# Kernel optimization log

Hardware: AMD Instinct MI355X
Metric: run time of the kernel (lower is better)

Reference implementation:

```python
import jax, jax.numpy as jnp
import numpy as np

SCALE = 1.0 / 8.0  # source divides sim_M by literal 8 (== sqrt(d_k=64))


def setup_inputs() -> dict:
    key = jax.random.key(0)
    ks = jax.random.split(key, 7)
    B, S, D = 16, 2048, 512  # D = n_head * d_k = 8 * 64
    s = 1.0 / np.sqrt(D)
    return {
        "x": jax.random.normal(ks[0], (B, S, D), dtype=jnp.float32),
        "Wq": jax.random.normal(ks[1], (D, D), dtype=jnp.float32) * s,
        "bq": jax.random.normal(ks[2], (D,), dtype=jnp.float32) * 0.01,
        "Wk": jax.random.normal(ks[3], (D, D), dtype=jnp.float32) * s,
        "bk": jax.random.normal(ks[4], (D,), dtype=jnp.float32) * 0.01,
        "Wv": jax.random.normal(ks[5], (D, D), dtype=jnp.float32) * s,
        "bv": jax.random.normal(ks[6], (D,), dtype=jnp.float32) * 0.01,
    }


def reference(x, Wq, bq, Wk, bk, Wv, bv):
    # Manual QKV projections (no head split, matching the source code)
    q = jnp.einsum("bsd,de->bse", x, Wq) + bq  # [B,S,D]
    k = jnp.einsum("bsd,de->bse", x, Wk) + bk  # [B,S,D]
    v = jnp.einsum("bsd,de->bse", x, Wv) + bv  # [B,S,D]
    # bmm -> softmax -> bmm attention
    sim = jnp.einsum("bqe,bke->bqk", q, k) * SCALE  # [B,S,S]
    attn = jax.nn.softmax(sim, axis=-1)
    out = jnp.einsum("bqk,bkd->bqd", attn, v)  # [B,S,D]
    return out
```

## Files before the change

kernel.cpp:

```cpp
#include <hip/hip_runtime.h>
#include <math.h>

typedef _Float16 f16;
typedef _Float16 f16x2 __attribute__((ext_vector_type(2)));
typedef _Float16 f16x8 __attribute__((ext_vector_type(8)));
typedef float f32x4 __attribute__((ext_vector_type(4)));

#define NB 16
#define SS 2048
#define DD 512

__device__ __forceinline__ void gl_lds16(const void* g, void* l) {
  __builtin_amdgcn_global_load_lds(
      (const __attribute__((address_space(1))) unsigned int*)g,
      (__attribute__((address_space(3))) unsigned int*)l, 16, 0, 0);
}

__device__ __forceinline__ int pk2(float a, float b) {
  f16x2 t = {(f16)a, (f16)b};
  return __builtin_bit_cast(int, t);
}

__global__ __launch_bounds__(256) void cast_kernel(const float* __restrict__ x,
                                                   f16* __restrict__ o) {
  size_t i = (size_t)blockIdx.x * 256 + threadIdx.x;
  const float4* p = (const float4*)x + i * 2;
  float4 a = p[0], b = p[1];
  f16x8 v = {(f16)a.x, (f16)a.y, (f16)a.z, (f16)a.w,
             (f16)b.x, (f16)b.y, (f16)b.z, (f16)b.w};
  *((f16x8*)o + i) = v;
}

__global__ __launch_bounds__(256) void transpose_kernel(
    const float* __restrict__ W0, const float* __restrict__ W1,
    const float* __restrict__ W2, f16* __restrict__ T0, f16* __restrict__ T1,
    f16* __restrict__ T2) {
  const float* W = (blockIdx.z == 0) ? W0 : (blockIdx.z == 1) ? W1 : W2;
  f16* Wt = (blockIdx.z == 0) ? T0 : (blockIdx.z == 1) ? T1 : T2;
  __shared__ float t[32][33];
  int bx = blockIdx.x * 32, by = blockIdx.y * 32;
  int c = threadIdx.x & 31, r0 = threadIdx.x >> 5;
  for (int r = r0; r < 32; r += 8) t[r][c] = W[(size_t)(by + r) * DD + bx + c];
  __syncthreads();
  for (int r = r0; r < 32; r += 8) Wt[(size_t)(bx + r) * DD + by + c] = (f16)t[c][r];
}

__global__ __launch_bounds__(256) void gemm3_kernel(
    const f16* __restrict__ xh, const f16* __restrict__ WqT,
    const f16* __restrict__ WkT, const f16* __restrict__ WvT,
    f16* __restrict__ Qh, f16* __restrict__ Kh, f16* __restrict__ Vth,
    const float* __restrict__ bq, const float* __restrict__ bk,
    const float* __restrict__ bv) {
  const int wid = (blockIdx.x & 7) * 384 + (blockIdx.x >> 3);
  const f16* A;
  const f16* Bt;
  f16* C;
  const float* bias;
  int m0, n0, ldc, bias_row;
  float scale;
  if (wid < 2048) {
    const bool isK = wid >= 1024;
    const int r = wid & 1023;
    A = xh;
    Bt = isK ? WkT : WqT;
    C = isK ? Kh : Qh;
    bias = isK ? bk : bq;
    m0 = (r >> 2) * 128;
    n0 = (r & 3) * 128;
    ldc = DD;
    bias_row = 0;
    scale = isK ? 1.0f : 0.125f;
  } else {
    const int v = wid - 2048;
    const int bz = v >> 6, xy = v & 63;
    A = WvT;
    Bt = xh + (size_t)bz * SS * DD;
    C = Vth + (size_t)bz * (size_t)DD * SS;
    bias = bv;
    m0 = ((xy >> 4) & 3) * 128;
    n0 = (xy & 15) * 128;
    ldc = SS;
    bias_row = 1;
    scale = 1.0f;
  }
  __shared__ f16 Ash[2][128 * 32];
  __shared__ f16 Bsh[2][128 * 32];
  const int tid = threadIdx.x, lane = tid & 63, wave = tid >> 6;
  const int wm = wave & 1, wn = wave >> 1;
  const int l15 = lane & 15, lq = lane >> 4;
  f32x4 acc[4][4] = {};
  const int srow = tid >> 2, part = tid & 3;
  const f16* gA = A + (size_t)(m0 + srow) * DD + part * 8;
  const f16* gB = Bt + (size_t)(n0 + srow) * DD + part * 8;
  auto stage = [&](int sb, int kt) {
    f16* lA = &Ash[sb][tid * 8];
    f16* lB = &Bsh[sb][tid * 8];
    gl_lds16(gA + kt * 32, lA);
    gl_lds16(gA + 64 * DD + kt * 32, lA + 2048);
    gl_lds16(gB + kt * 32, lB);
    gl_lds16(gB + 64 * DD + kt * 32, lB + 2048);
  };
  stage(0, 0);
  __syncthreads();
  for (int kt = 0; kt < 16; ++kt) {
    const int buf = kt & 1;
    if (kt < 15) stage(buf ^ 1, kt + 1);
    f16x8 af[4], bf[4];
#pragma unroll
    for (int i = 0; i < 4; ++i)
      af[i] = *(const f16x8*)&Ash[buf][(64 * wm + 16 * i + l15) * 32 + lq * 8];
#pragma unroll
    for (int j = 0; j < 4; ++j)
      bf[j] = *(const f16x8*)&Bsh[buf][(64 * wn + 16 * j + l15) * 32 + lq * 8];
#pragma unroll
    for (int i = 0; i < 4; ++i)
#pragma unroll
      for (int j = 0; j < 4; ++j)
        acc[i][j] = __builtin_amdgcn_mfma_f32_16x16x32_f16(af[i], bf[j], acc[i][j], 0, 0, 0);
    __syncthreads();
  }
#pragma unroll
  for (int i = 0; i < 4; ++i) {
    int rb = 64 * wm + 16 * i + lq * 4;
#pragma unroll
    for (int j = 0; j < 4; ++j) {
      int cc = n0 + 64 * wn + 16 * j + l15;
#pragma unroll
      for (int r = 0; r < 4; ++r) {
        int rr = m0 + rb + r;
        float bv = bias_row ? bias[rr] : bias[cc];
        C[(size_t)rr * ldc + cc] = (f16)((acc[i][j][r] + bv) * scale);
      }
    }
  }
}

__global__ __launch_bounds__(512, 2) void attn_kernel(
    const f16* __restrict__ Q, const f16* __restrict__ K,
    const f16* __restrict__ Vt, float* __restrict__ out) {
  const int id = blockIdx.x;
  const int b = (id & 7) + ((id >> 7) << 3);
  const int qt = (id >> 3) & 15;
  const int tid = threadIdx.x, lane = tid & 63, wave = tid >> 6;
  const int l15 = lane & 15, lq = lane >> 4;

  __shared__ __align__(16) f16 Kl[2][32][520];
  __shared__ __align__(16) f16 Vl[2][512][32];

  const f16* qp = Q + ((size_t)(b * SS + qt * 128 + wave * 16 + l15)) * DD + lq * 8;
  f16x8 qf[16];
#pragma unroll
  for (int kk = 0; kk < 16; ++kk) qf[kk] = *(const f16x8*)(qp + kk * 32);

  const f16* Kb = K + (size_t)b * SS * DD;
  const f16* Vb = Vt + (size_t)b * DD * SS;

  const int sdata = (lane & 3) ^ ((lane >> 3) & 3);
  const int vrow = lane >> 2;
  const int vs_off = (lq ^ ((l15 >> 1) & 3)) * 8;

  f16x8 onef;
#pragma unroll
  for (int j = 0; j < 8; ++j) onef[j] = (f16)1.0f;

  auto stage = [&](int sb, int kb) {
#pragma unroll
    for (int rr = 0; rr < 4; ++rr) {
      int row = wave * 4 + rr;
      gl_lds16(Kb + ((size_t)(kb + row)) * DD + lane * 8, &Kl[sb][row][lane * 8]);
    }
#pragma unroll
    for (int i = 0; i < 4; ++i) {
      int e0 = wave * 64 + i * 16;
      gl_lds16(Vb + (size_t)(e0 + vrow) * SS + kb + sdata * 8,
               (f16*)&Vl[sb][e0][0] + lane * 8);
    }
  };

  stage(0, 0);
  __syncthreads();

  f32x4 acco[32] = {};
  f32x4 accl = {};
  float m = -1e30f;

  for (int it = 0; it < 64; ++it) {
    const int buf = it & 1;
    if (it < 63) stage(buf ^ 1, (it + 1) * 32);
    f32x4 sa0 = {}, sa1 = {};
#pragma unroll
    for (int kk = 0; kk < 16; ++kk) {
      f16x8 b0 = *(const f16x8*)&Kl[buf][l15][kk * 32 + lq * 8];
      f16x8 b1 = *(const f16x8*)&Kl[buf][16 + l15][kk * 32 + lq * 8];
      sa0 = __builtin_amdgcn_mfma_f32_16x16x32_f16(b0, qf[kk], sa0, 0, 0, 0);
      sa1 = __builtin_amdgcn_mfma_f32_16x16x32_f16(b1, qf[kk], sa1, 0, 0, 0);
    }
    float lm = fmaxf(fmaxf(fmaxf(sa0[0], sa0[1]), fmaxf(sa0[2], sa0[3])),
                     fmaxf(fmaxf(sa1[0], sa1[1]), fmaxf(sa1[2], sa1[3])));
    if (__any(lm > m + 8.0f)) {
      float mx = lm;
      mx = fmaxf(mx, __shfl_xor(mx, 16));
      mx = fmaxf(mx, __shfl_xor(mx, 32));
      float mn = fmaxf(m, mx);
      float al = __expf(m - mn);
      m = mn;
      float alr[4];
#pragma unroll
      for (int r = 0; r < 4; ++r) alr[r] = __shfl(al, 4 * lq + r);
#pragma unroll
      for (int t = 0; t < 32; ++t)
#pragma unroll
        for (int r = 0; r < 4; ++r) acco[t][r] *= alr[r];
#pragma unroll
      for (int r = 0; r < 4; ++r) accl[r] *= alr[r];
    }
    int A0 = pk2(__expf(sa0[0] - m), __expf(sa0[1] - m));
    int A1 = pk2(__expf(sa0[2] - m), __expf(sa0[3] - m));
    int B0 = pk2(__expf(sa1[0] - m), __expf(sa1[1] - m));
    int B1 = pk2(__expf(sa1[2] - m), __expf(sa1[3] - m));
    const bool low = (lq < 2);
    int s0 = low ? B0 : A0, s1 = low ? B1 : A1;
    int X0 = __shfl_xor(s0, 32), X1 = __shfl_xor(s1, 32);
    int Y0 = low ? A0 : B0, Y1 = low ? A1 : B1;
    const bool sx = (lq == 0) || (lq == 3);
    int t0 = sx ? X0 : Y0, t1 = sx ? X1 : Y1;
    int Z0 = __shfl_xor(t0, 16), Z1 = __shfl_xor(t1, 16);
    union PU { int i[4]; f16x8 v; } pu;
    pu.i[0] = (lq == 0) ? Y0 : ((lq == 2) ? X0 : Z0);
    pu.i[1] = (lq == 0) ? Y1 : ((lq == 2) ? X1 : Z1);
    pu.i[2] = (lq == 1) ? X0 : ((lq == 3) ? Y0 : Z0);
    pu.i[3] = (lq == 1) ? X1 : ((lq == 3) ? Y1 : Z1);
    f16x8 pa = pu.v;
    accl = __builtin_amdgcn_mfma_f32_16x16x32_f16(pa, onef, accl, 0, 0, 0);
#pragma unroll
    for (int nn = 0; nn < 32; ++nn) {
      f16x8 vf = *(const f16x8*)&Vl[buf][nn * 16 + l15][vs_off];
      acco[nn] = __builtin_amdgcn_mfma_f32_16x16x32_f16(pa, vf, acco[nn], 0, 0, 0);
    }
    __syncthreads();
  }
  float inv[4];
#pragma unroll
  for (int r = 0; r < 4; ++r) inv[r] = 1.0f / accl[r];
  const size_t ob = ((size_t)(b * SS + qt * 128 + wave * 16 + 4 * lq)) * DD + l15;
#pragma unroll
  for (int nn = 0; nn < 32; ++nn)
#pragma unroll
    for (int r = 0; r < 4; ++r)
      out[ob + (size_t)r * DD + nn * 16] = acco[nn][r] * inv[r];
}

extern "C" void kernel_launch(void* const* d_in, const int* in_sizes, int n_in,
                              void* d_out, int out_size, void* d_ws, size_t ws_size,
                              hipStream_t stream) {
  const float* x = (const float*)d_in[0];
  const float* Wq = (const float*)d_in[1];
  const float* bq = (const float*)d_in[2];
  const float* Wk = (const float*)d_in[3];
  const float* bk = (const float*)d_in[4];
  const float* Wv = (const float*)d_in[5];
  const float* bv = (const float*)d_in[6];
  float* out = (float*)d_out;
  f16* ws = (f16*)d_ws;
  const size_t NX = (size_t)NB * SS * DD;
  f16* xh = ws;
  f16* Qh = ws + NX;
  f16* Kh = ws + 2 * NX;
  f16* Vth = ws + 3 * NX;
  f16* WqT = ws + 4 * NX;
  f16* WkT = WqT + DD * DD;
  f16* WvT = WkT + DD * DD;

  cast_kernel<<<NX / 8 / 256, 256, 0, stream>>>(x, xh);
  transpose_kernel<<<dim3(16, 16, 3), 256, 0, stream>>>(Wq, Wk, Wv, WqT, WkT, WvT);
  gemm3_kernel<<<3072, 256, 0, stream>>>(xh, WqT, WkT, WvT, Qh, Kh, Vth, bq, bk, bv);
  attn_kernel<<<256, 512, 0, stream>>>(Qh, Kh, Vth, out);
}
```

Measured before the change: 395.3 us.

## Enlarge QKV projection GEMM tiles to 256x256 with XOR-swizzled LDS

The QKV projection GEMM now uses 256x256 output tiles computed by 512-thread blocks, with a K-step of 64 and 8x4 MFMA accumulators per wave, launching 768 blocks instead of 3072 128x128 blocks. LDS staging uses an XOR swizzle on 16-byte segments to avoid bank conflicts. The V path swaps operand roles so it can share the same staged tiles. The goal is more data reuse per LDS load and fewer global loads. The cost is 128 KB of LDS per block and higher register pressure, which lowers occupancy, and fewer blocks for the GPU's compute units.

```diff
diff --git a/kernel.cpp b/kernel.cpp
--- a/kernel.cpp
+++ b/kernel.cpp
@@ -45,91 +45,105 @@
   for (int r = r0; r < 32; r += 8) Wt[(size_t)(bx + r) * DD + by + c] = (f16)t[c][r];
 }
 
-__global__ __launch_bounds__(256) void gemm3_kernel(
+__global__ __launch_bounds__(512, 2) void gemmQKV_kernel(
     const f16* __restrict__ xh, const f16* __restrict__ WqT,
     const f16* __restrict__ WkT, const f16* __restrict__ WvT,
     f16* __restrict__ Qh, f16* __restrict__ Kh, f16* __restrict__ Vth,
     const float* __restrict__ bq, const float* __restrict__ bk,
     const float* __restrict__ bv) {
-  const int wid = (blockIdx.x & 7) * 384 + (blockIdx.x >> 3);
-  const f16* A;
-  const f16* Bt;
+  const int wid = (blockIdx.x & 7) * 96 + (blockIdx.x >> 3);
+  const f16* Wm;
   f16* C;
   const float* bias;
-  int m0, n0, ldc, bias_row;
+  size_t x0;
+  size_t crow0, ccol0;
+  int w0, ldc, bias_row;
   float scale;
-  if (wid < 2048) {
-    const bool isK = wid >= 1024;
-    const int r = wid & 1023;
-    A = xh;
-    Bt = isK ? WkT : WqT;
+  bool isV;
+  if (wid < 512) {
+    const bool isK = wid >= 256;
+    const int r = wid & 255;
+    x0 = (size_t)(r >> 1) * 256;
+    w0 = (r & 1) * 256;
+    Wm = isK ? WkT : WqT;
     C = isK ? Kh : Qh;
     bias = isK ? bk : bq;
-    m0 = (r >> 2) * 128;
-    n0 = (r & 3) * 128;
+    crow0 = x0;
+    ccol0 = (size_t)w0;
     ldc = DD;
     bias_row = 0;
     scale = isK ? 1.0f : 0.125f;
+    isV = false;
   } else {
-    const int v = wid - 2048;
-    const int bz = v >> 6, xy = v & 63;
-    A = WvT;
-    Bt = xh + (size_t)bz * SS * DD;
-    C = Vth + (size_t)bz * (size_t)DD * SS;
+    const int v = wid - 512;
+    const int b = v >> 4, e = (v >> 3) & 1, s = v & 7;
+    x0 = (size_t)b * SS + (size_t)s * 256;
+    w0 = e * 256;
+    Wm = WvT;
+    C = Vth + (size_t)b * DD * SS;
     bias = bv;
-    m0 = ((xy >> 4) & 3) * 128;
-    n0 = (xy & 15) * 128;
+    crow0 = (size_t)w0;
+    ccol0 = (size_t)s * 256;
     ldc = SS;
     bias_row = 1;
     scale = 1.0f;
-  }
-  __shared__ f16 Ash[2][128 * 32];
-  __shared__ f16 Bsh[2][128 * 32];
+    isV = true;
+  }
+  __shared__ f16 Xsh[2][256][64];
+  __shared__ f16 Wsh[2][256][64];
   const int tid = threadIdx.x, lane = tid & 63, wave = tid >> 6;
-  const int wm = wave & 1, wn = wave >> 1;
+  const int wm2 = wave >> 2, wn2 = wave & 3;
   const int l15 = lane & 15, lq = lane >> 4;
-  f32x4 acc[4][4] = {};
-  const int srow = tid >> 2, part = tid & 3;
-  const f16* gA = A + (size_t)(m0 + srow) * DD + part * 8;
-  const f16* gB = Bt + (size_t)(n0 + srow) * DD + part * 8;
+  const int srow = lane >> 3;
+  const int sseg = (lane & 7) ^ srow;
+  f32x4 acc[8][4] = {};
   auto stage = [&](int sb, int kt) {
-    f16* lA = &Ash[sb][tid * 8];
-    f16* lB = &Bsh[sb][tid * 8];
-    gl_lds16(gA + kt * 32, lA);
-    gl_lds16(gA + 64 * DD + kt * 32, lA + 2048);
-    gl_lds16(gB + kt * 32, lB);
-    gl_lds16(gB + 64 * DD + kt * 32, lB + 2048);
+#pragma unroll
+    for (int g = 0; g < 4; ++g) {
+      const int r0 = wave * 32 + g * 8;
+      gl_lds16(xh + (x0 + r0 + srow) * DD + kt * 64 + sseg * 8,
+               (f16*)&Xsh[sb][r0][0] + lane * 8);
+      gl_lds16(Wm + (size_t)(w0 + r0 + srow) * DD + kt * 64 + sseg * 8,
+               (f16*)&Wsh[sb][r0][0] + lane * 8);
+    }
   };
   stage(0, 0);
   __syncthreads();
-  for (int kt = 0; kt < 16; ++kt) {
+  for (int kt = 0; kt < 8; ++kt) {
     const int buf = kt & 1;
-    if (kt < 15) stage(buf ^ 1, kt + 1);
-    f16x8 af[4], bf[4];
-#pragma unroll
-    for (int i = 0; i < 4; ++i)
-      af[i] = *(const f16x8*)&Ash[buf][(64 * wm + 16 * i + l15) * 32 + lq * 8];
-#pragma unroll
-    for (int j = 0; j < 4; ++j)
-      bf[j] = *(const f16x8*)&Bsh[buf][(64 * wn + 16 * j + l15) * 32 + lq * 8];
-#pragma unroll
-    for (int i = 0; i < 4; ++i)
+    if (kt < 7) stage(buf ^ 1, kt + 1);
+    const f16(*As)[64] = isV ? Wsh[buf] : Xsh[buf];
+    const f16(*Bs)[64] = isV ? Xsh[buf] : Wsh[buf];
+#pragma unroll
+    for (int kk = 0; kk < 2; ++kk) {
+      const int seg = (((kk * 4 + lq) ^ (l15 & 7))) * 8;
+      f16x8 af[8], bf[4];
+#pragma unroll
+      for (int i = 0; i < 8; ++i)
+        af[i] = *(const f16x8*)&As[128 * wm2 + 16 * i + l15][seg];
 #pragma unroll
       for (int j = 0; j < 4; ++j)
-        acc[i][j] = __builtin_amdgcn_mfma_f32_16x16x32_f16(af[i], bf[j], acc[i][j], 0, 0, 0);
+        bf[j] = *(const f16x8*)&Bs[64 * wn2 + 16 * j + l15][seg];
+#pragma unroll
+      for (int i = 0; i < 8; ++i)
+#pragma unroll
+        for (int j = 0; j < 4; ++j)
+          acc[i][j] = __builtin_amdgcn_mfma_f32_16x16x32_f16(af[i], bf[j], acc[i][j], 0, 0, 0);
+    }
     __syncthreads();
   }
 #pragma unroll
-  for (int i = 0; i < 4; ++i) {
-    int rb = 64 * wm + 16 * i + lq * 4;
+  for (int i = 0; i < 8; ++i) {
+    const int arow = 128 * wm2 + 16 * i + 4 * lq;
 #pragma unroll
     for (int j = 0; j < 4; ++j) {
-      int cc = n0 + 64 * wn + 16 * j + l15;
+      const int acol = 64 * wn2 + 16 * j + l15;
 #pragma unroll
       for (int r = 0; r < 4; ++r) {
-        int rr = m0 + rb + r;
-        float bv = bias_row ? bias[rr] : bias[cc];
-        C[(size_t)rr * ldc + cc] = (f16)((acc[i][j][r] + bv) * scale);
+        const size_t rr = crow0 + arow + r;
+        const size_t cc = ccol0 + acol;
+        const float bvv = bias_row ? bias[rr] : bias[cc];
+        C[rr * ldc + cc] = (f16)((acc[i][j][r] + bvv) * scale);
       }
     }
   }
@@ -273,6 +287,6 @@
 
   cast_kernel<<<NX / 8 / 256, 256, 0, stream>>>(x, xh);
   transpose_kernel<<<dim3(16, 16, 3), 256, 0, stream>>>(Wq, Wk, Wv, WqT, WkT, WvT);
-  gemm3_kernel<<<3072, 256, 0, stream>>>(xh, WqT, WkT, WvT, Qh, Kh, Vth, bq, bk, bv);
+  gemmQKV_kernel<<<768, 512, 0, stream>>>(xh, WqT, WkT, WvT, Qh, Kh, Vth, bq, bk, bv);
   attn_kernel<<<256, 512, 0, stream>>>(Qh, Kh, Vth, out);
 }
```

After: 408.8 us. 1.03x slower.

## Split PV accumulation by output columns per wave, sharing P through LDS

Applied to the files above, without the earlier changes.

Each wave now owns a 64-column slice of the output for all 128 query rows instead of all 512 columns for its own 16 rows. Softmax probabilities, rescale factors and trigger flags are exchanged through shared memory with an extra barrier per iteration. Each wave reads only its four V fragments from LDS, not all 32, which cuts LDS traffic for V. The cost is an added barrier, LDS writes and reads of P from every wave, and per-wave rescale branches.

```diff
diff --git a/kernel.cpp b/kernel.cpp
--- a/kernel.cpp
+++ b/kernel.cpp
@@ -146,6 +146,9 @@
 
   __shared__ __align__(16) f16 Kl[2][32][520];
   __shared__ __align__(16) f16 Vl[2][512][32];
+  __shared__ __align__(16) f16 Pash[8][512];
+  __shared__ __align__(16) float alsh[128];
+  __shared__ __align__(16) int flg[8];
 
   const f16* qp = Q + ((size_t)(b * SS + qt * 128 + wave * 16 + l15)) * DD + lq * 8;
   f16x8 qf[16];
@@ -180,7 +183,7 @@
   stage(0, 0);
   __syncthreads();
 
-  f32x4 acco[32] = {};
+  f32x4 acco[8][4] = {};
   f32x4 accl = {};
   float m = -1e30f;
 
@@ -197,9 +200,9 @@
     }
     float lm = fmaxf(fmaxf(fmaxf(sa0[0], sa0[1]), fmaxf(sa0[2], sa0[3])),
                      fmaxf(fmaxf(sa1[0], sa1[1]), fmaxf(sa1[2], sa1[3])));
-    if (__any(lm > m + 8.0f)) {
-      float mx = lm;
-      mx = fmaxf(mx, __shfl_xor(mx, 16));
+    const bool trig = __any(lm > m + 8.0f);
+    if (trig) {
+      float mx = fmaxf(lm, __shfl_xor(lm, 16));
       mx = fmaxf(mx, __shfl_xor(mx, 32));
       float mn = fmaxf(m, mx);
       float al = __expf(m - mn);
@@ -208,12 +211,10 @@
 #pragma unroll
       for (int r = 0; r < 4; ++r) alr[r] = __shfl(al, 4 * lq + r);
 #pragma unroll
-      for (int t = 0; t < 32; ++t)
-#pragma unroll
-        for (int r = 0; r < 4; ++r) acco[t][r] *= alr[r];
-#pragma unroll
       for (int r = 0; r < 4; ++r) accl[r] *= alr[r];
-    }
+      if (lq == 0) alsh[wave * 16 + l15] = al;
+    }
+    if (lane == 0) flg[wave] = trig ? 1 : 0;
     int A0 = pk2(__expf(sa0[0] - m), __expf(sa0[1] - m));
     int A1 = pk2(__expf(sa0[2] - m), __expf(sa0[3] - m));
     int B0 = pk2(__expf(sa1[0] - m), __expf(sa1[1] - m));
@@ -232,22 +233,48 @@
     pu.i[3] = (lq == 1) ? X1 : ((lq == 3) ? Y1 : Z1);
     f16x8 pa = pu.v;
     accl = __builtin_amdgcn_mfma_f32_16x16x32_f16(pa, onef, accl, 0, 0, 0);
-#pragma unroll
-    for (int nn = 0; nn < 32; ++nn) {
-      f16x8 vf = *(const f16x8*)&Vl[buf][nn * 16 + l15][vs_off];
-      acco[nn] = __builtin_amdgcn_mfma_f32_16x16x32_f16(pa, vf, acco[nn], 0, 0, 0);
+    *(f16x8*)&Pash[wave][lane * 8] = pa;
+    asm volatile("s_waitcnt lgkmcnt(0)" ::: "memory");
+    __builtin_amdgcn_s_barrier();
+    __builtin_amdgcn_sched_barrier(0);
+    int4 f0 = *(const int4*)&flg[0];
+    int4 f4 = *(const int4*)&flg[4];
+    const int fl[8] = {f0.x, f0.y, f0.z, f0.w, f4.x, f4.y, f4.z, f4.w};
+    f16x8 vf[4];
+#pragma unroll
+    for (int j = 0; j < 4; ++j)
+      vf[j] = *(const f16x8*)&Vl[buf][wave * 64 + j * 16 + l15][vs_off];
+#pragma unroll
+    for (int t = 0; t < 8; ++t) {
+      if (fl[t]) {
+        f32x4 alv = *(const f32x4*)&alsh[t * 16 + lq * 4];
+#pragma unroll
+        for (int j = 0; j < 4; ++j)
+#pragma unroll
+          for (int r = 0; r < 4; ++r) acco[t][j][r] *= alv[r];
+      }
+      f16x8 paT = *(const f16x8*)&Pash[t][lane * 8];
+#pragma unroll
+      for (int j = 0; j < 4; ++j)
+        acco[t][j] = __builtin_amdgcn_mfma_f32_16x16x32_f16(paT, vf[j], acco[t][j], 0, 0, 0);
     }
     __syncthreads();
   }
-  float inv[4];
-#pragma unroll
-  for (int r = 0; r < 4; ++r) inv[r] = 1.0f / accl[r];
-  const size_t ob = ((size_t)(b * SS + qt * 128 + wave * 16 + 4 * lq)) * DD + l15;
-#pragma unroll
-  for (int nn = 0; nn < 32; ++nn)
-#pragma unroll
-    for (int r = 0; r < 4; ++r)
-      out[ob + (size_t)r * DD + nn * 16] = acco[nn][r] * inv[r];
+  if (l15 == 0) {
+    f32x4 iv = {1.0f / accl[0], 1.0f / accl[1], 1.0f / accl[2], 1.0f / accl[3]};
+    *(f32x4*)&alsh[wave * 16 + lq * 4] = iv;
+  }
+  __syncthreads();
+  const size_t ob = (size_t)(b * SS + qt * 128) * DD + wave * 64 + l15;
+#pragma unroll
+  for (int t = 0; t < 8; ++t) {
+    f32x4 iv = *(const f32x4*)&alsh[t * 16 + lq * 4];
+#pragma unroll
+    for (int j = 0; j < 4; ++j)
+#pragma unroll
+      for (int r = 0; r < 4; ++r)
+        out[ob + (size_t)(t * 16 + 4 * lq + r) * DD + j * 16] = acco[t][j][r] * iv[r];
+  }
 }
 
 extern "C" void kernel_launch(void* const* d_in, const int* in_sizes, int n_in,
```

New measurement: 440.4 us. 11.4% more time.
